# Kernel tuning notes

Measured on AMD Instinct MI355X. Metric: run time of the kernel, lower is better.

The kernel has to match this reference:

```python
import jax, jax.numpy as jnp
import numpy as np

INPUT_DIM, HIDDEN, LATENT, HEADS = 4, 32, 2, 4
N_NODES, N_EDGES = 50000, 800000
EPS_BN = 1e-5
NEG_SLOPE = 0.2


def _glorot(key, shape):
    fan_in, fan_out = shape[0], shape[-1]
    lim = jnp.sqrt(6.0 / (fan_in + fan_out))
    return jax.random.uniform(key, shape, jnp.float32, -lim, lim)


def setup_inputs() -> dict:
    key = jax.random.key(0)
    ks = jax.random.split(key, 20)
    x = jax.random.normal(ks[0], (N_NODES, INPUT_DIM), jnp.float32)
    edge_index = jax.random.randint(ks[1], (2, N_EDGES), 0, N_NODES, jnp.int64)

    def gat_params(k, in_ch, out_ch, heads, concat):
        k1, k2, k3 = jax.random.split(k, 3)
        W = _glorot(k1, (in_ch, heads * out_ch))
        a_src = _glorot(k2, (heads, out_ch))
        a_dst = _glorot(k3, (heads, out_ch))
        b = jnp.zeros((heads * out_ch,) if concat else (out_ch,), jnp.float32)
        return W, a_src, a_dst, b

    w_e1, as_e1, ad_e1, b_e1 = gat_params(ks[2], INPUT_DIM, HIDDEN, HEADS, True)
    w_e3, as_e3, ad_e3, b_e3 = gat_params(ks[3], HIDDEN * HEADS, LATENT, 1, False)
    w_d1, as_d1, ad_d1, b_d1 = gat_params(ks[4], LATENT, HIDDEN, HEADS, True)
    w_d3, as_d3, ad_d3, b_d3 = gat_params(ks[5], HIDDEN * HEADS, INPUT_DIM, 1, False)

    return dict(
        x=x, edge_index=edge_index,
        bn_gamma=jnp.ones((INPUT_DIM,), jnp.float32),
        bn_beta=jnp.zeros((INPUT_DIM,), jnp.float32),
        w_e1=w_e1, as_e1=as_e1, ad_e1=ad_e1, b_e1=b_e1,
        w_e3=w_e3, as_e3=as_e3, ad_e3=ad_e3, b_e3=b_e3,
        w_d1=w_d1, as_d1=as_d1, ad_d1=ad_d1, b_d1=b_d1,
        w_d3=w_d3, as_d3=as_d3, ad_d3=ad_d3, b_d3=b_d3,
    )


def gat_conv(x, src, dst, W, a_src, a_dst, b, heads, out_ch, concat):
    """PyG-style GATConv: gather -> attention -> segment softmax -> scatter."""
    n = x.shape[0]
    h = (x @ W).reshape(n, heads, out_ch)                 # [N,H,C]
    alpha_s = jnp.sum(h * a_src, axis=-1)                 # [N,H]
    alpha_d = jnp.sum(h * a_dst, axis=-1)                 # [N,H]
    e = jax.nn.leaky_relu(alpha_s[src] + alpha_d[dst], NEG_SLOPE)  # [E,H]
    # numerically-stable softmax over incoming edges of each dst node
    m = jax.ops.segment_max(e, dst, num_segments=n)
    e = jnp.exp(e - m[dst])
    s = jax.ops.segment_sum(e, dst, num_segments=n)
    a = e / (s[dst] + 1e-16)                              # [E,H]
    msg = h[src] * a[:, :, None]                          # [E,H,C]
    out = jax.ops.segment_sum(msg, dst, num_segments=n)   # [N,H,C]
    out = out.reshape(n, heads * out_ch) if concat else out.mean(axis=1)
    return out + b


def reference(x, edge_index, bn_gamma, bn_beta,
              w_e1, as_e1, ad_e1, b_e1,
              w_e3, as_e3, ad_e3, b_e3,
              w_d1, as_d1, ad_d1, b_d1,
              w_d3, as_d3, ad_d3, b_d3):
    n = x.shape[0]
    # GATConv default add_self_loops=True
    loops = jnp.arange(n, dtype=edge_index.dtype)
    src = jnp.concatenate([edge_index[0], loops])
    dst = jnp.concatenate([edge_index[1], loops])

    # BatchNorm1d (training-mode batch statistics, biased variance)
    mu = x.mean(axis=0)
    var = x.var(axis=0)
    x_in = (x - mu) * jax.lax.rsqrt(var + EPS_BN) * bn_gamma + bn_beta

    enc1 = jax.nn.relu(gat_conv(x_in, src, dst, w_e1, as_e1, ad_e1, b_e1, HEADS, HIDDEN, True))
    latent = gat_conv(enc1, src, dst, w_e3, as_e3, ad_e3, b_e3, 1, LATENT, False)
    dec1 = jax.nn.relu(gat_conv(latent, src, dst, w_d1, as_d1, ad_d1, b_d1, HEADS, HIDDEN, True))
    x_out = gat_conv(dec1, src, dst, w_d3, as_d3, ad_d3, b_d3, 1, INPUT_DIM, False)
    return x_out
```

## Files before the change

### kernel.cpp

```cpp
#include <hip/hip_runtime.h>

#define NN 50000
#define E0 800000
#define ET 850000
#define EPS_BN 1e-5f
#define SLOPE 0.2f
#define NBP 32
#define EPC 2048
#define NCH 416
#define PBITS 10
#define NP 49
#define SCN (NP*NCH)

__device__ __forceinline__ float lrelu(float v){ return v > 0.f ? v : SLOPE*v; }

__global__ __launch_bounds__(256) void chunk_hist_bn(const int* __restrict__ ei, int* __restrict__ chunkcnt,
                                                     const float* __restrict__ x, float* __restrict__ part){
  __shared__ int cc[NP];
  for (int i=threadIdx.x; i<NP; i+=256) cc[i]=0;
  __syncthreads();
  int base = blockIdx.x*EPC;
  int end = min(base+EPC, ET);
  for (int e = base+threadIdx.x; e < end; e += 256){
    int dst = (e < E0) ? ei[E0 + e] : (e - E0);
    atomicAdd(&cc[dst>>PBITS], 1);
  }
  __syncthreads();
  for (int i=threadIdx.x; i<NP; i+=256) chunkcnt[blockIdx.x*NP + i] = cc[i];

  if (blockIdx.x < NBP){
    float s[4]={0,0,0,0}, q[4]={0,0,0,0};
    for (int n = blockIdx.x*256 + threadIdx.x; n < NN; n += NBP*256){
      float4 v = reinterpret_cast<const float4*>(x)[n];
      s[0]+=v.x; s[1]+=v.y; s[2]+=v.z; s[3]+=v.w;
      q[0]+=v.x*v.x; q[1]+=v.y*v.y; q[2]+=v.z*v.z; q[3]+=v.w*v.w;
    }
    #pragma unroll
    for (int m=1;m<64;m<<=1){
      #pragma unroll
      for (int i=0;i<4;i++){ s[i]+=__shfl_xor(s[i],m); q[i]+=__shfl_xor(q[i],m); }
    }
    __shared__ float lds[4][8];
    int wid = threadIdx.x>>6, lane = threadIdx.x&63;
    if (lane==0){
      #pragma unroll
      for (int i=0;i<4;i++){ lds[wid][i]=s[i]; lds[wid][4+i]=q[i]; }
    }
    __syncthreads();
    if (threadIdx.x < 8){
      float p = lds[0][threadIdx.x]+lds[1][threadIdx.x]+lds[2][threadIdx.x]+lds[3][threadIdx.x];
      part[blockIdx.x*8 + threadIdx.x] = p;
    }
  }
}

__global__ __launch_bounds__(1024) void scan_fold(
    const int* __restrict__ chunkcnt, int* __restrict__ pofs,
    const float* __restrict__ part, const float* __restrict__ gamma, const float* __restrict__ beta,
    const float* __restrict__ w_e1, const float* __restrict__ as_e1, const float* __restrict__ ad_e1,
    const float* __restrict__ w_d1, const float* __restrict__ as_d1, const float* __restrict__ ad_d1,
    float* __restrict__ sclsft, float* __restrict__ fold){
  __shared__ int wsum[1024];
  int t = threadIdx.x;
  const int PER = (SCN + 1023)/1024;
  int vals[PER];
  int mysum = 0;
  #pragma unroll
  for (int k=0;k<PER;k++){
    int idx = t*PER + k;
    int v = 0;
    if (idx < SCN){ int p = idx/NCH, ch = idx - p*NCH; v = chunkcnt[ch*NP + p]; }
    vals[k] = v; mysum += v;
  }
  wsum[t] = mysum; __syncthreads();
  int val = mysum;
  for (int off=1; off<1024; off<<=1){
    int tmp = (t>=off) ? wsum[t-off] : 0;
    __syncthreads();
    val += tmp; wsum[t] = val; __syncthreads();
  }
  int run = val - mysum;
  #pragma unroll
  for (int k=0;k<PER;k++){
    int idx = t*PER + k;
    if (idx < SCN){ int p = idx/NCH, ch = idx - p*NCH; pofs[ch*NP + p] = run; }
    run += vals[k];
  }

  if (t < 64){
    int ch = t&7, bslot = t>>3;
    float s = 0.f;
    for (int b=bslot; b<NBP; b+=8) s += part[b*8 + ch];
    s += __shfl_xor(s,8); s += __shfl_xor(s,16); s += __shfl_xor(s,32);
    float qv = __shfl(s, (t&3)+4);
    if (t < 4){
      float mu  = s*(1.0f/NN);
      float var = qv*(1.0f/NN) - mu*mu;
      float scl = rsqrtf(var + EPS_BN)*gamma[t];
      sclsft[t]   = scl;
      sclsft[4+t] = beta[t] - mu*scl;
    }
  } else if (t < 128){
    int u = t - 64;
    if (u < 32){
      int idx = u & 15; int h = idx>>2; int i = idx&3;
      const float* a = (u<16) ? as_e1 : ad_e1;
      float sum = 0.f;
      for (int c=0;c<32;c++) sum += w_e1[i*128 + h*32 + c] * a[h*32 + c];
      fold[u] = sum;
    } else if (u < 48){
      int idx = u - 32; int j = idx & 7; int h = j>>1; int i = j&1;
      const float* a = (idx<8) ? as_d1 : ad_d1;
      float sum = 0.f;
      for (int c=0;c<32;c++) sum += w_d1[i*128 + h*32 + c] * a[h*32 + c];
      fold[32 + idx] = sum;
    }
  }
}

__global__ __launch_bounds__(256) void partition_pass(const int* __restrict__ ei,
                                                      const int* __restrict__ pofs,
                                                      int2* __restrict__ pedge){
  __shared__ int cur[NP];
  for (int i=threadIdx.x; i<NP; i+=256) cur[i] = pofs[blockIdx.x*NP + i];
  __syncthreads();
  int base = blockIdx.x*EPC;
  int end = min(base+EPC, ET);
  for (int e = base+threadIdx.x; e < end; e += 256){
    int src, dst;
    if (e < E0){ src = ei[e]; dst = ei[E0+e]; } else { src = dst = e - E0; }
    int pos = atomicAdd(&cur[dst>>PBITS], 1);
    pedge[pos] = make_int2(src, dst);
  }
}

__global__ __launch_bounds__(1024) void fine_build(const int2* __restrict__ pedge,
                                                   const int* __restrict__ pofs,
                                                   int* __restrict__ rowptr, int* __restrict__ ssrc){
  int p = blockIdx.x;
  int pstart = pofs[p];
  int pend = (p+1 < NP) ? pofs[p+1] : ET;
  int dbase = p << PBITS;
  __shared__ int hist[1<<PBITS];
  __shared__ int cur[1<<PBITS];
  int t = threadIdx.x;
  hist[t] = 0;
  __syncthreads();
  for (int i = pstart + t; i < pend; i += 1024)
    atomicAdd(&hist[pedge[i].y - dbase], 1);
  __syncthreads();
  int orig = hist[t];
  __syncthreads();
  int v = orig;
  for (int off=1; off<1024; off<<=1){
    int tmp = (t>=off) ? hist[t-off] : 0;
    __syncthreads();
    v += tmp; hist[t] = v; __syncthreads();
  }
  int excl = v - orig;
  int d = dbase + t;
  if (d < NN) rowptr[d] = pstart + excl;
  if (p == NP-1 && t == 0) rowptr[NN] = ET;
  cur[t] = pstart + excl;
  __syncthreads();
  for (int i = pstart + t; i < pend; i += 1024){
    int2 e = pedge[i];
    int pos = atomicAdd(&cur[e.y - dbase], 1);
    ssrc[pos] = e.x;
  }
}

__global__ __launch_bounds__(256) void node1(
    const float* __restrict__ x, const float* __restrict__ sclsft, const float* __restrict__ fold,
    float* __restrict__ pk1, float* __restrict__ ald1){
  int n = blockIdx.x*256 + threadIdx.x;
  if (n >= NN) return;
  float4 v = reinterpret_cast<const float4*>(x)[n];
  float xb[4] = {v.x, v.y, v.z, v.w};
  #pragma unroll
  for (int i=0;i<4;i++) xb[i] = xb[i]*sclsft[i] + sclsft[4+i];
  float4 s4, d4;
  float* sp = &s4.x; float* dp = &d4.x;
  #pragma unroll
  for (int h=0;h<4;h++){
    float s=0.f, d=0.f;
    #pragma unroll
    for (int i=0;i<4;i++){ s += xb[i]*fold[h*4+i]; d += xb[i]*fold[16+h*4+i]; }
    sp[h]=s; dp[h]=d;
  }
  reinterpret_cast<float4*>(pk1)[n*2+0] = s4;
  reinterpret_cast<float4*>(pk1)[n*2+1] = make_float4(xb[0],xb[1],xb[2],xb[3]);
  reinterpret_cast<float4*>(ald1)[n] = d4;
}

__global__ __launch_bounds__(256) void eagg1(
    const float* __restrict__ pk1, const float* __restrict__ ald,
    const int* __restrict__ rowptr, const int* __restrict__ ssrc,
    const float* __restrict__ w_e1, const float* __restrict__ b_e1,
    const float* __restrict__ w_e3, const float* __restrict__ as_e3, const float* __restrict__ ad_e3,
    float* __restrict__ pk2, float* __restrict__ ald2){
  int dst = blockIdx.x*32 + (threadIdx.x>>3);
  int sub = threadIdx.x & 7;
  if (dst >= NN) return;
  int r0 = rowptr[dst], r1 = rowptr[dst+1];
  float4 advv = reinterpret_cast<const float4*>(ald)[dst];
  float adv[4] = {advv.x, advv.y, advv.z, advv.w};
  float sum[4] = {0,0,0,0};
  float acc[4][4] = {{0,0,0,0},{0,0,0,0},{0,0,0,0},{0,0,0,0}};
  for (int i = r0 + sub; i < r1; i += 8){
    int s = ssrc[i];
    float4 a = reinterpret_cast<const float4*>(pk1)[s*2+0];
    float4 f = reinterpret_cast<const float4*>(pk1)[s*2+1];
    float av[4] = {a.x,a.y,a.z,a.w};
    #pragma unroll
    for (int h=0;h<4;h++){
      float w = __expf(lrelu(av[h]+adv[h]));
      sum[h] += w;
      acc[h][0] += w*f.x; acc[h][1] += w*f.y; acc[h][2] += w*f.z; acc[h][3] += w*f.w;
    }
  }
  #pragma unroll
  for (int m=1;m<8;m<<=1){
    #pragma unroll
    for (int h=0;h<4;h++){
      sum[h] += __shfl_xor(sum[h],m);
      #pragma unroll
      for (int c=0;c<4;c++) acc[h][c] += __shfl_xor(acc[h][c],m);
    }
  }
  int hh = sub>>1;
  float G0=acc[0][0], G1=acc[0][1], G2=acc[0][2], G3=acc[0][3], GS=sum[0];
  #pragma unroll
  for (int h=1;h<4;h++){
    if (hh==h){ G0=acc[h][0]; G1=acc[h][1]; G2=acc[h][2]; G3=acc[h][3]; GS=sum[h]; }
  }
  float ginv = 1.f/(GS+1e-16f);
  G0*=ginv; G1*=ginv; G2*=ginv; G3*=ginv;
  float p0 = 0.f, p1 = 0.f;
  int ocb = sub*16;
  #pragma unroll
  for (int q=0;q<4;q++){
    int o = ocb + q*4;
    float4 b  = *reinterpret_cast<const float4*>(b_e1 + o);
    float4 w0 = *reinterpret_cast<const float4*>(w_e1 + 0*128 + o);
    float4 w1 = *reinterpret_cast<const float4*>(w_e1 + 1*128 + o);
    float4 w2 = *reinterpret_cast<const float4*>(w_e1 + 2*128 + o);
    float4 w3 = *reinterpret_cast<const float4*>(w_e1 + 3*128 + o);
    float e0 = fmaxf(b.x + G0*w0.x + G1*w1.x + G2*w2.x + G3*w3.x, 0.f);
    float e1 = fmaxf(b.y + G0*w0.y + G1*w1.y + G2*w2.y + G3*w3.y, 0.f);
    float e2 = fmaxf(b.z + G0*w0.z + G1*w1.z + G2*w2.z + G3*w3.z, 0.f);
    float e3 = fmaxf(b.w + G0*w0.w + G1*w1.w + G2*w2.w + G3*w3.w, 0.f);
    float4 wa = *reinterpret_cast<const float4*>(w_e3 + o*2);
    float4 wb = *reinterpret_cast<const float4*>(w_e3 + o*2 + 4);
    p0 += e0*wa.x + e1*wa.z + e2*wb.x + e3*wb.z;
    p1 += e0*wa.y + e1*wa.w + e2*wb.y + e3*wb.w;
  }
  #pragma unroll
  for (int m=1;m<8;m<<=1){ p0 += __shfl_xor(p0,m); p1 += __shfl_xor(p1,m); }
  if (sub==0){
    reinterpret_cast<float4*>(pk2)[dst] = make_float4(p0, p1, p0*as_e3[0]+p1*as_e3[1], 0.f);
    ald2[dst] = p0*ad_e3[0] + p1*ad_e3[1];
  }
}

__global__ __launch_bounds__(256) void eagg2(
    const float* __restrict__ pk2, const float* __restrict__ ald2,
    const int* __restrict__ rowptr, const int* __restrict__ ssrc,
    const float* __restrict__ b_e3, const float* __restrict__ fold,
    float* __restrict__ pk3, float* __restrict__ ald3){
  int dst = blockIdx.x*32 + (threadIdx.x>>3);
  int sub = threadIdx.x & 7;
  if (dst >= NN) return;
  int r0 = rowptr[dst], r1 = rowptr[dst+1];
  float adv = ald2[dst];
  float sum = 0.f, a0 = 0.f, a1 = 0.f;
  for (int i = r0 + sub; i < r1; i += 8){
    int s = ssrc[i];
    float4 r = reinterpret_cast<const float4*>(pk2)[s];
    float w = __expf(lrelu(r.z + adv));
    sum += w; a0 += w*r.x; a1 += w*r.y;
  }
  #pragma unroll
  for (int m=1;m<8;m<<=1){
    sum += __shfl_xor(sum,m); a0 += __shfl_xor(a0,m); a1 += __shfl_xor(a1,m);
  }
  if (sub != 0) return;
  float inv = 1.f/(sum+1e-16f);
  float l0 = a0*inv + b_e3[0];
  float l1 = a1*inv + b_e3[1];
  float4 s3, d3; float* sp=&s3.x; float* dp=&d3.x;
  #pragma unroll
  for (int h=0;h<4;h++){
    sp[h] = l0*fold[32+h*2+0] + l1*fold[32+h*2+1];
    dp[h] = l0*fold[40+h*2+0] + l1*fold[40+h*2+1];
  }
  reinterpret_cast<float4*>(pk3)[dst*2] = s3;
  pk3[(size_t)dst*8+4] = l0;
  pk3[(size_t)dst*8+5] = l1;
  reinterpret_cast<float4*>(ald3)[dst] = d3;
}

__global__ __launch_bounds__(256) void eagg3(
    const float* __restrict__ pk3, const float* __restrict__ ald3,
    const int* __restrict__ rowptr, const int* __restrict__ ssrc,
    const float* __restrict__ w_d1, const float* __restrict__ b_d1,
    const float* __restrict__ w_d3, const float* __restrict__ as_d3, const float* __restrict__ ad_d3,
    float4* __restrict__ feat4, float* __restrict__ s4a, float* __restrict__ ald4){
  int dst = blockIdx.x*32 + (threadIdx.x>>3);
  int sub = threadIdx.x & 7;
  if (dst >= NN) return;
  int r0 = rowptr[dst], r1 = rowptr[dst+1];
  float4 advv = reinterpret_cast<const float4*>(ald3)[dst];
  float adv[4] = {advv.x, advv.y, advv.z, advv.w};
  float sum[4] = {0,0,0,0};
  float acc[4][2] = {{0,0},{0,0},{0,0},{0,0}};
  for (int i = r0 + sub; i < r1; i += 8){
    int s = ssrc[i];
    float4 a = reinterpret_cast<const float4*>(pk3)[s*2+0];
    float2 f = *reinterpret_cast<const float2*>(pk3 + (size_t)s*8 + 4);
    float av[4] = {a.x,a.y,a.z,a.w};
    #pragma unroll
    for (int h=0;h<4;h++){
      float w = __expf(lrelu(av[h]+adv[h]));
      sum[h] += w;
      acc[h][0] += w*f.x; acc[h][1] += w*f.y;
    }
  }
  #pragma unroll
  for (int m=1;m<8;m<<=1){
    #pragma unroll
    for (int h=0;h<4;h++){
      sum[h] += __shfl_xor(sum[h],m);
      acc[h][0] += __shfl_xor(acc[h][0],m);
      acc[h][1] += __shfl_xor(acc[h][1],m);
    }
  }
  int hh = sub>>1;
  float G0=acc[0][0], G1=acc[0][1], GS=sum[0];
  #pragma unroll
  for (int h=1;h<4;h++){
    if (hh==h){ G0=acc[h][0]; G1=acc[h][1]; GS=sum[h]; }
  }
  float ginv = 1.f/(GS+1e-16f);
  G0*=ginv; G1*=ginv;
  float p0=0.f,p1=0.f,p2=0.f,p3=0.f;
  int ocb = sub*16;
  #pragma unroll
  for (int q=0;q<4;q++){
    int o = ocb + q*4;
    float4 b  = *reinterpret_cast<const float4*>(b_d1 + o);
    float4 w0 = *reinterpret_cast<const float4*>(w_d1 + 0*128 + o);
    float4 w1 = *reinterpret_cast<const float4*>(w_d1 + 1*128 + o);
    float e0 = fmaxf(b.x + G0*w0.x + G1*w1.x, 0.f);
    float e1 = fmaxf(b.y + G0*w0.y + G1*w1.y, 0.f);
    float e2 = fmaxf(b.z + G0*w0.z + G1*w1.z, 0.f);
    float e3 = fmaxf(b.w + G0*w0.w + G1*w1.w, 0.f);
    float4 d0 = *reinterpret_cast<const float4*>(w_d3 + (o+0)*4);
    float4 d1 = *reinterpret_cast<const float4*>(w_d3 + (o+1)*4);
    float4 d2 = *reinterpret_cast<const float4*>(w_d3 + (o+2)*4);
    float4 d3v = *reinterpret_cast<const float4*>(w_d3 + (o+3)*4);
    p0 += e0*d0.x + e1*d1.x + e2*d2.x + e3*d3v.x;
    p1 += e0*d0.y + e1*d1.y + e2*d2.y + e3*d3v.y;
    p2 += e0*d0.z + e1*d1.z + e2*d2.z + e3*d3v.z;
    p3 += e0*d0.w + e1*d1.w + e2*d2.w + e3*d3v.w;
  }
  #pragma unroll
  for (int m=1;m<8;m<<=1){
    p0 += __shfl_xor(p0,m); p1 += __shfl_xor(p1,m);
    p2 += __shfl_xor(p2,m); p3 += __shfl_xor(p3,m);
  }
  if (sub==0){
    feat4[dst] = make_float4(p0,p1,p2,p3);
    s4a[dst]  = p0*as_d3[0]+p1*as_d3[1]+p2*as_d3[2]+p3*as_d3[3];
    ald4[dst] = p0*ad_d3[0]+p1*ad_d3[1]+p2*ad_d3[2]+p3*ad_d3[3];
  }
}

__global__ __launch_bounds__(256) void eagg4(
    const float4* __restrict__ feat4, const float* __restrict__ s4a, const float* __restrict__ ald4,
    const int* __restrict__ rowptr, const int* __restrict__ ssrc,
    const float* __restrict__ b_d3, float* __restrict__ out){
  int dst = blockIdx.x*32 + (threadIdx.x>>3);
  int sub = threadIdx.x & 7;
  if (dst >= NN) return;
  int r0 = rowptr[dst], r1 = rowptr[dst+1];
  float adv = ald4[dst];
  float sum = 0.f, a0=0.f, a1=0.f, a2=0.f, a3=0.f;
  for (int i = r0 + sub; i < r1; i += 8){
    int s = ssrc[i];
    float w = __expf(lrelu(s4a[s] + adv));
    float4 f = feat4[s];
    sum += w; a0 += w*f.x; a1 += w*f.y; a2 += w*f.z; a3 += w*f.w;
  }
  #pragma unroll
  for (int m=1;m<8;m<<=1){
    sum += __shfl_xor(sum,m);
    a0 += __shfl_xor(a0,m); a1 += __shfl_xor(a1,m);
    a2 += __shfl_xor(a2,m); a3 += __shfl_xor(a3,m);
  }
  if (sub != 0) return;
  float inv = 1.f/(sum+1e-16f);
  reinterpret_cast<float4*>(out)[dst] =
    make_float4(a0*inv+b_d3[0], a1*inv+b_d3[1], a2*inv+b_d3[2], a3*inv+b_d3[3]);
}

extern "C" void kernel_launch(void* const* d_in, const int* in_sizes, int n_in,
                              void* d_out, int out_size, void* d_ws, size_t ws_size,
                              hipStream_t stream) {
  const float* x     = (const float*)d_in[0];
  const int*   ei    = (const int*)  d_in[1];
  const float* gamma = (const float*)d_in[2];
  const float* beta  = (const float*)d_in[3];
  const float* w_e1  = (const float*)d_in[4];
  const float* as_e1 = (const float*)d_in[5];
  const float* ad_e1 = (const float*)d_in[6];
  const float* b_e1  = (const float*)d_in[7];
  const float* w_e3  = (const float*)d_in[8];
  const float* as_e3 = (const float*)d_in[9];
  const float* ad_e3 = (const float*)d_in[10];
  const float* b_e3  = (const float*)d_in[11];
  const float* w_d1  = (const float*)d_in[12];
  const float* as_d1 = (const float*)d_in[13];
  const float* ad_d1 = (const float*)d_in[14];
  const float* b_d1  = (const float*)d_in[15];
  const float* w_d3  = (const float*)d_in[16];
  const float* as_d3 = (const float*)d_in[17];
  const float* ad_d3 = (const float*)d_in[18];
  const float* b_d3  = (const float*)d_in[19];

  char* ws = (char*)d_ws;
  size_t off = 0;
  auto alloc = [&](size_t bytes)->void*{
    void* p = ws + off;
    off += (bytes + 255) & ~(size_t)255;
    return p;
  };
  int*   chunkcnt = (int*)  alloc((size_t)NCH*NP*4);
  int*   pofs     = (int*)  alloc((size_t)NCH*NP*4);
  int2*  pedge    = (int2*) alloc((size_t)ET*8);
  int*   rowptr   = (int*)  alloc((size_t)(NN+1)*4);
  int*   ssrc     = (int*)  alloc((size_t)ET*4);
  float* part     = (float*)alloc((size_t)NBP*8*4);
  float* sclsft   = (float*)alloc(32);
  float* fold     = (float*)alloc(64*4);
  float* pk1      = (float*)alloc((size_t)NN*8*4);
  float* ald1     = (float*)alloc((size_t)NN*4*4);
  float* pk2      = (float*)alloc((size_t)NN*4*4);
  float* ald2     = (float*)alloc((size_t)NN*4);
  float* pk3      = (float*)alloc((size_t)NN*8*4);
  float* ald3     = (float*)alloc((size_t)NN*4*4);
  float4* feat4   = (float4*)alloc((size_t)NN*4*4);
  float* s4a      = (float*)alloc((size_t)NN*4);
  float* ald4     = (float*)alloc((size_t)NN*4);

  chunk_hist_bn<<<NCH, 256, 0, stream>>>(ei, chunkcnt, x, part);
  scan_fold<<<1, 1024, 0, stream>>>(chunkcnt, pofs, part, gamma, beta,
                                    w_e1, as_e1, ad_e1, w_d1, as_d1, ad_d1, sclsft, fold);
  partition_pass<<<NCH, 256, 0, stream>>>(ei, pofs, pedge);
  fine_build<<<NP, 1024, 0, stream>>>(pedge, pofs, rowptr, ssrc);

  const int AGG_BLOCKS = (NN+31)/32;

  node1<<<(NN+255)/256, 256, 0, stream>>>(x, sclsft, fold, pk1, ald1);
  eagg1<<<AGG_BLOCKS, 256, 0, stream>>>(pk1, ald1, rowptr, ssrc,
                                        w_e1, b_e1, w_e3, as_e3, ad_e3, pk2, ald2);
  eagg2<<<AGG_BLOCKS, 256, 0, stream>>>(pk2, ald2, rowptr, ssrc, b_e3, fold, pk3, ald3);
  eagg3<<<AGG_BLOCKS, 256, 0, stream>>>(pk3, ald3, rowptr, ssrc,
                                        w_d1, b_d1, w_d3, as_d3, ad_d3, feat4, s4a, ald4);
  eagg4<<<AGG_BLOCKS, 256, 0, stream>>>(feat4, s4a, ald4, rowptr, ssrc, b_d3, (float*)d_out);
}
```

Measured before the change: 127.9 us.

## Drop node1 pass, recompute attention logits on the fly, narrow gather records

Removes the node1 kernel. eagg1 now gathers raw x and applies the batch-norm scale and the folded attention vectors per edge, and later layers store only compact features (float2/float4) while recomputing source and destination logits from them. This cuts per-edge gather bytes and intermediate writes, at the cost of some extra per-edge arithmetic. It also retunes the CSR build to larger chunks, 1024-thread blocks and 512-node partitions, and uses 4 lanes per destination node in place of 8.

Result: faster. 124.1 us (-3.0%).

```diff
diff --git a/kernel.cpp b/kernel.cpp
--- a/kernel.cpp
+++ b/kernel.cpp
@@ -6,31 +6,32 @@
 #define EPS_BN 1e-5f
 #define SLOPE 0.2f
 #define NBP 32
-#define EPC 2048
-#define NCH 416
-#define PBITS 10
-#define NP 49
+#define EPC 8192
+#define NCH 104
+#define PBITS 9
+#define NP 98
 #define SCN (NP*NCH)
 
 __device__ __forceinline__ float lrelu(float v){ return v > 0.f ? v : SLOPE*v; }
 
-__global__ __launch_bounds__(256) void chunk_hist_bn(const int* __restrict__ ei, int* __restrict__ chunkcnt,
-                                                     const float* __restrict__ x, float* __restrict__ part){
+__global__ __launch_bounds__(1024) void chunk_hist_bn(const int* __restrict__ ei, int* __restrict__ chunkcnt,
+                                                      const float* __restrict__ x, float* __restrict__ part){
   __shared__ int cc[NP];
-  for (int i=threadIdx.x; i<NP; i+=256) cc[i]=0;
+  int t = threadIdx.x;
+  for (int i=t; i<NP; i+=1024) cc[i]=0;
   __syncthreads();
   int base = blockIdx.x*EPC;
   int end = min(base+EPC, ET);
-  for (int e = base+threadIdx.x; e < end; e += 256){
+  for (int e = base+t; e < end; e += 1024){
     int dst = (e < E0) ? ei[E0 + e] : (e - E0);
     atomicAdd(&cc[dst>>PBITS], 1);
   }
   __syncthreads();
-  for (int i=threadIdx.x; i<NP; i+=256) chunkcnt[blockIdx.x*NP + i] = cc[i];
+  for (int i=t; i<NP; i+=1024) chunkcnt[blockIdx.x*NP + i] = cc[i];
 
   if (blockIdx.x < NBP){
     float s[4]={0,0,0,0}, q[4]={0,0,0,0};
-    for (int n = blockIdx.x*256 + threadIdx.x; n < NN; n += NBP*256){
+    for (int n = blockIdx.x*1024 + t; n < NN; n += NBP*1024){
       float4 v = reinterpret_cast<const float4*>(x)[n];
       s[0]+=v.x; s[1]+=v.y; s[2]+=v.z; s[3]+=v.w;
       q[0]+=v.x*v.x; q[1]+=v.y*v.y; q[2]+=v.z*v.z; q[3]+=v.w*v.w;
@@ -40,16 +41,18 @@
       #pragma unroll
       for (int i=0;i<4;i++){ s[i]+=__shfl_xor(s[i],m); q[i]+=__shfl_xor(q[i],m); }
     }
-    __shared__ float lds[4][8];
-    int wid = threadIdx.x>>6, lane = threadIdx.x&63;
+    __shared__ float lds[16][8];
+    int wid = t>>6, lane = t&63;
     if (lane==0){
       #pragma unroll
       for (int i=0;i<4;i++){ lds[wid][i]=s[i]; lds[wid][4+i]=q[i]; }
     }
     __syncthreads();
-    if (threadIdx.x < 8){
-      float p = lds[0][threadIdx.x]+lds[1][threadIdx.x]+lds[2][threadIdx.x]+lds[3][threadIdx.x];
-      part[blockIdx.x*8 + threadIdx.x] = p;
+    if (t < 8){
+      float p = 0.f;
+      #pragma unroll
+      for (int w=0;w<16;w++) p += lds[w][t];
+      part[blockIdx.x*8 + t] = p;
     }
   }
 }
@@ -118,15 +121,16 @@
   }
 }
 
-__global__ __launch_bounds__(256) void partition_pass(const int* __restrict__ ei,
-                                                      const int* __restrict__ pofs,
-                                                      int2* __restrict__ pedge){
+__global__ __launch_bounds__(1024) void partition_pass(const int* __restrict__ ei,
+                                                       const int* __restrict__ pofs,
+                                                       int2* __restrict__ pedge){
   __shared__ int cur[NP];
-  for (int i=threadIdx.x; i<NP; i+=256) cur[i] = pofs[blockIdx.x*NP + i];
+  int t = threadIdx.x;
+  for (int i=t; i<NP; i+=1024) cur[i] = pofs[blockIdx.x*NP + i];
   __syncthreads();
   int base = blockIdx.x*EPC;
   int end = min(base+EPC, ET);
-  for (int e = base+threadIdx.x; e < end; e += 256){
+  for (int e = base+t; e < end; e += 1024){
     int src, dst;
     if (e < E0){ src = ei[e]; dst = ei[E0+e]; } else { src = dst = e - E0; }
     int pos = atomicAdd(&cur[dst>>PBITS], 1);
@@ -144,24 +148,27 @@
   __shared__ int hist[1<<PBITS];
   __shared__ int cur[1<<PBITS];
   int t = threadIdx.x;
-  hist[t] = 0;
+  if (t < 512) hist[t] = 0;
   __syncthreads();
   for (int i = pstart + t; i < pend; i += 1024)
     atomicAdd(&hist[pedge[i].y - dbase], 1);
   __syncthreads();
-  int orig = hist[t];
+  int orig = (t < 512) ? hist[t] : 0;
   __syncthreads();
   int v = orig;
-  for (int off=1; off<1024; off<<=1){
-    int tmp = (t>=off) ? hist[t-off] : 0;
+  for (int off=1; off<512; off<<=1){
+    int tmp = (t>=off && t<512) ? hist[t-off] : 0;
     __syncthreads();
-    v += tmp; hist[t] = v; __syncthreads();
-  }
-  int excl = v - orig;
-  int d = dbase + t;
-  if (d < NN) rowptr[d] = pstart + excl;
-  if (p == NP-1 && t == 0) rowptr[NN] = ET;
-  cur[t] = pstart + excl;
+    if (t < 512){ v += tmp; hist[t] = v; }
+    __syncthreads();
+  }
+  if (t < 512){
+    int excl = v - orig;
+    int d = dbase + t;
+    if (d < NN) rowptr[d] = pstart + excl;
+    if (p == NP-1 && t == 0) rowptr[NN] = ET;
+    cur[t] = pstart + excl;
+  }
   __syncthreads();
   for (int i = pstart + t; i < pend; i += 1024){
     int2 e = pedge[i];
@@ -170,57 +177,44 @@
   }
 }
 
-__global__ __launch_bounds__(256) void node1(
+__global__ __launch_bounds__(256) void eagg1(
     const float* __restrict__ x, const float* __restrict__ sclsft, const float* __restrict__ fold,
-    float* __restrict__ pk1, float* __restrict__ ald1){
-  int n = blockIdx.x*256 + threadIdx.x;
-  if (n >= NN) return;
-  float4 v = reinterpret_cast<const float4*>(x)[n];
-  float xb[4] = {v.x, v.y, v.z, v.w};
-  #pragma unroll
-  for (int i=0;i<4;i++) xb[i] = xb[i]*sclsft[i] + sclsft[4+i];
-  float4 s4, d4;
-  float* sp = &s4.x; float* dp = &d4.x;
-  #pragma unroll
-  for (int h=0;h<4;h++){
-    float s=0.f, d=0.f;
-    #pragma unroll
-    for (int i=0;i<4;i++){ s += xb[i]*fold[h*4+i]; d += xb[i]*fold[16+h*4+i]; }
-    sp[h]=s; dp[h]=d;
-  }
-  reinterpret_cast<float4*>(pk1)[n*2+0] = s4;
-  reinterpret_cast<float4*>(pk1)[n*2+1] = make_float4(xb[0],xb[1],xb[2],xb[3]);
-  reinterpret_cast<float4*>(ald1)[n] = d4;
-}
-
-__global__ __launch_bounds__(256) void eagg1(
-    const float* __restrict__ pk1, const float* __restrict__ ald,
     const int* __restrict__ rowptr, const int* __restrict__ ssrc,
-    const float* __restrict__ w_e1, const float* __restrict__ b_e1,
-    const float* __restrict__ w_e3, const float* __restrict__ as_e3, const float* __restrict__ ad_e3,
-    float* __restrict__ pk2, float* __restrict__ ald2){
-  int dst = blockIdx.x*32 + (threadIdx.x>>3);
-  int sub = threadIdx.x & 7;
+    const float* __restrict__ w_e1, const float* __restrict__ b_e1, const float* __restrict__ w_e3,
+    float2* __restrict__ pk2){
+  int dst = blockIdx.x*64 + (threadIdx.x>>2);
+  int sub = threadIdx.x & 3;
   if (dst >= NN) return;
+  float sc[8];
+  #pragma unroll
+  for (int i=0;i<8;i++) sc[i] = sclsft[i];
+  float fs[16];
+  #pragma unroll
+  for (int i=0;i<16;i++) fs[i] = fold[i];
+  float4 xd = reinterpret_cast<const float4*>(x)[dst];
+  float xbd[4] = {xd.x*sc[0]+sc[4], xd.y*sc[1]+sc[5], xd.z*sc[2]+sc[6], xd.w*sc[3]+sc[7]};
+  float ald[4];
+  #pragma unroll
+  for (int h=0;h<4;h++)
+    ald[h] = xbd[0]*fold[16+h*4+0] + xbd[1]*fold[16+h*4+1]
+           + xbd[2]*fold[16+h*4+2] + xbd[3]*fold[16+h*4+3];
   int r0 = rowptr[dst], r1 = rowptr[dst+1];
-  float4 advv = reinterpret_cast<const float4*>(ald)[dst];
-  float adv[4] = {advv.x, advv.y, advv.z, advv.w};
   float sum[4] = {0,0,0,0};
   float acc[4][4] = {{0,0,0,0},{0,0,0,0},{0,0,0,0},{0,0,0,0}};
-  for (int i = r0 + sub; i < r1; i += 8){
+  for (int i = r0 + sub; i < r1; i += 4){
     int s = ssrc[i];
-    float4 a = reinterpret_cast<const float4*>(pk1)[s*2+0];
-    float4 f = reinterpret_cast<const float4*>(pk1)[s*2+1];
-    float av[4] = {a.x,a.y,a.z,a.w};
+    float4 xs = reinterpret_cast<const float4*>(x)[s];
+    float xb[4] = {xs.x*sc[0]+sc[4], xs.y*sc[1]+sc[5], xs.z*sc[2]+sc[6], xs.w*sc[3]+sc[7]};
     #pragma unroll
     for (int h=0;h<4;h++){
-      float w = __expf(lrelu(av[h]+adv[h]));
+      float a = xb[0]*fs[h*4+0] + xb[1]*fs[h*4+1] + xb[2]*fs[h*4+2] + xb[3]*fs[h*4+3];
+      float w = __expf(lrelu(a + ald[h]));
       sum[h] += w;
-      acc[h][0] += w*f.x; acc[h][1] += w*f.y; acc[h][2] += w*f.z; acc[h][3] += w*f.w;
-    }
-  }
-  #pragma unroll
-  for (int m=1;m<8;m<<=1){
+      acc[h][0] += w*xb[0]; acc[h][1] += w*xb[1]; acc[h][2] += w*xb[2]; acc[h][3] += w*xb[3];
+    }
+  }
+  #pragma unroll
+  for (int m=1;m<4;m<<=1){
     #pragma unroll
     for (int h=0;h<4;h++){
       sum[h] += __shfl_xor(sum[h],m);
@@ -228,19 +222,18 @@
       for (int c=0;c<4;c++) acc[h][c] += __shfl_xor(acc[h][c],m);
     }
   }
-  int hh = sub>>1;
   float G0=acc[0][0], G1=acc[0][1], G2=acc[0][2], G3=acc[0][3], GS=sum[0];
   #pragma unroll
   for (int h=1;h<4;h++){
-    if (hh==h){ G0=acc[h][0]; G1=acc[h][1]; G2=acc[h][2]; G3=acc[h][3]; GS=sum[h]; }
-  }
-  float ginv = 1.f/(GS+1e-16f);
-  G0*=ginv; G1*=ginv; G2*=ginv; G3*=ginv;
+    if (sub==h){ G0=acc[h][0]; G1=acc[h][1]; G2=acc[h][2]; G3=acc[h][3]; GS=sum[h]; }
+  }
+  float inv = 1.f/(GS+1e-16f);
+  G0*=inv; G1*=inv; G2*=inv; G3*=inv;
   float p0 = 0.f, p1 = 0.f;
-  int ocb = sub*16;
-  #pragma unroll
-  for (int q=0;q<4;q++){
-    int o = ocb + q*4;
+  int ob = sub*32;
+  #pragma unroll
+  for (int q=0;q<8;q++){
+    int o = ob + q*4;
     float4 b  = *reinterpret_cast<const float4*>(b_e1 + o);
     float4 w0 = *reinterpret_cast<const float4*>(w_e1 + 0*128 + o);
     float4 w1 = *reinterpret_cast<const float4*>(w_e1 + 1*128 + o);
@@ -255,79 +248,71 @@
     p0 += e0*wa.x + e1*wa.z + e2*wb.x + e3*wb.z;
     p1 += e0*wa.y + e1*wa.w + e2*wb.y + e3*wb.w;
   }
-  #pragma unroll
-  for (int m=1;m<8;m<<=1){ p0 += __shfl_xor(p0,m); p1 += __shfl_xor(p1,m); }
+  p0 += __shfl_xor(p0,1); p0 += __shfl_xor(p0,2);
+  p1 += __shfl_xor(p1,1); p1 += __shfl_xor(p1,2);
+  if (sub==0) pk2[dst] = make_float2(p0, p1);
+}
+
+__global__ __launch_bounds__(256) void eagg2(
+    const float2* __restrict__ pk2,
+    const int* __restrict__ rowptr, const int* __restrict__ ssrc,
+    const float* __restrict__ as_e3, const float* __restrict__ ad_e3, const float* __restrict__ b_e3,
+    float2* __restrict__ lat2){
+  int dst = blockIdx.x*64 + (threadIdx.x>>2);
+  int sub = threadIdx.x & 3;
+  if (dst >= NN) return;
+  float as0 = as_e3[0], as1 = as_e3[1];
+  float2 pd = pk2[dst];
+  float adv = pd.x*ad_e3[0] + pd.y*ad_e3[1];
+  int r0 = rowptr[dst], r1 = rowptr[dst+1];
+  float sum = 0.f, a0 = 0.f, a1 = 0.f;
+  for (int i = r0 + sub; i < r1; i += 4){
+    int s = ssrc[i];
+    float2 p = pk2[s];
+    float w = __expf(lrelu(p.x*as0 + p.y*as1 + adv));
+    sum += w; a0 += w*p.x; a1 += w*p.y;
+  }
+  #pragma unroll
+  for (int m=1;m<4;m<<=1){
+    sum += __shfl_xor(sum,m); a0 += __shfl_xor(a0,m); a1 += __shfl_xor(a1,m);
+  }
   if (sub==0){
-    reinterpret_cast<float4*>(pk2)[dst] = make_float4(p0, p1, p0*as_e3[0]+p1*as_e3[1], 0.f);
-    ald2[dst] = p0*ad_e3[0] + p1*ad_e3[1];
-  }
-}
-
-__global__ __launch_bounds__(256) void eagg2(
-    const float* __restrict__ pk2, const float* __restrict__ ald2,
+    float inv = 1.f/(sum+1e-16f);
+    lat2[dst] = make_float2(a0*inv + b_e3[0], a1*inv + b_e3[1]);
+  }
+}
+
+__global__ __launch_bounds__(256) void eagg3(
+    const float2* __restrict__ lat2, const float* __restrict__ fold,
     const int* __restrict__ rowptr, const int* __restrict__ ssrc,
-    const float* __restrict__ b_e3, const float* __restrict__ fold,
-    float* __restrict__ pk3, float* __restrict__ ald3){
-  int dst = blockIdx.x*32 + (threadIdx.x>>3);
-  int sub = threadIdx.x & 7;
+    const float* __restrict__ w_d1, const float* __restrict__ b_d1, const float* __restrict__ w_d3,
+    float4* __restrict__ pk4){
+  int dst = blockIdx.x*64 + (threadIdx.x>>2);
+  int sub = threadIdx.x & 3;
   if (dst >= NN) return;
+  float f3[8];
+  #pragma unroll
+  for (int i=0;i<8;i++) f3[i] = fold[32+i];
+  float2 ld = lat2[dst];
+  float ald[4];
+  #pragma unroll
+  for (int h=0;h<4;h++) ald[h] = ld.x*fold[40+h*2+0] + ld.y*fold[40+h*2+1];
   int r0 = rowptr[dst], r1 = rowptr[dst+1];
-  float adv = ald2[dst];
-  float sum = 0.f, a0 = 0.f, a1 = 0.f;
-  for (int i = r0 + sub; i < r1; i += 8){
-    int s = ssrc[i];
-    float4 r = reinterpret_cast<const float4*>(pk2)[s];
-    float w = __expf(lrelu(r.z + adv));
-    sum += w; a0 += w*r.x; a1 += w*r.y;
-  }
-  #pragma unroll
-  for (int m=1;m<8;m<<=1){
-    sum += __shfl_xor(sum,m); a0 += __shfl_xor(a0,m); a1 += __shfl_xor(a1,m);
-  }
-  if (sub != 0) return;
-  float inv = 1.f/(sum+1e-16f);
-  float l0 = a0*inv + b_e3[0];
-  float l1 = a1*inv + b_e3[1];
-  float4 s3, d3; float* sp=&s3.x; float* dp=&d3.x;
-  #pragma unroll
-  for (int h=0;h<4;h++){
-    sp[h] = l0*fold[32+h*2+0] + l1*fold[32+h*2+1];
-    dp[h] = l0*fold[40+h*2+0] + l1*fold[40+h*2+1];
-  }
-  reinterpret_cast<float4*>(pk3)[dst*2] = s3;
-  pk3[(size_t)dst*8+4] = l0;
-  pk3[(size_t)dst*8+5] = l1;
-  reinterpret_cast<float4*>(ald3)[dst] = d3;
-}
-
-__global__ __launch_bounds__(256) void eagg3(
-    const float* __restrict__ pk3, const float* __restrict__ ald3,
-    const int* __restrict__ rowptr, const int* __restrict__ ssrc,
-    const float* __restrict__ w_d1, const float* __restrict__ b_d1,
-    const float* __restrict__ w_d3, const float* __restrict__ as_d3, const float* __restrict__ ad_d3,
-    float4* __restrict__ feat4, float* __restrict__ s4a, float* __restrict__ ald4){
-  int dst = blockIdx.x*32 + (threadIdx.x>>3);
-  int sub = threadIdx.x & 7;
-  if (dst >= NN) return;
-  int r0 = rowptr[dst], r1 = rowptr[dst+1];
-  float4 advv = reinterpret_cast<const float4*>(ald3)[dst];
-  float adv[4] = {advv.x, advv.y, advv.z, advv.w};
   float sum[4] = {0,0,0,0};
   float acc[4][2] = {{0,0},{0,0},{0,0},{0,0}};
-  for (int i = r0 + sub; i < r1; i += 8){
+  for (int i = r0 + sub; i < r1; i += 4){
     int s = ssrc[i];
-    float4 a = reinterpret_cast<const float4*>(pk3)[s*2+0];
-    float2 f = *reinterpret_cast<const float2*>(pk3 + (size_t)s*8 + 4);
-    float av[4] = {a.x,a.y,a.z,a.w};
+    float2 l = lat2[s];
     #pragma unroll
     for (int h=0;h<4;h++){
-      float w = __expf(lrelu(av[h]+adv[h]));
+      float a = l.x*f3[h*2+0] + l.y*f3[h*2+1];
+      float w = __expf(lrelu(a + ald[h]));
       sum[h] += w;
-      acc[h][0] += w*f.x; acc[h][1] += w*f.y;
-    }
-  }
-  #pragma unroll
-  for (int m=1;m<8;m<<=1){
+      acc[h][0] += w*l.x; acc[h][1] += w*l.y;
+    }
+  }
+  #pragma unroll
+  for (int m=1;m<4;m<<=1){
     #pragma unroll
     for (int h=0;h<4;h++){
       sum[h] += __shfl_xor(sum[h],m);
@@ -335,19 +320,18 @@
       acc[h][1] += __shfl_xor(acc[h][1],m);
     }
   }
-  int hh = sub>>1;
   float G0=acc[0][0], G1=acc[0][1], GS=sum[0];
   #pragma unroll
   for (int h=1;h<4;h++){
-    if (hh==h){ G0=acc[h][0]; G1=acc[h][1]; GS=sum[h]; }
-  }
-  float ginv = 1.f/(GS+1e-16f);
-  G0*=ginv; G1*=ginv;
+    if (sub==h){ G0=acc[h][0]; G1=acc[h][1]; GS=sum[h]; }
+  }
+  float inv = 1.f/(GS+1e-16f);
+  G0*=inv; G1*=inv;
   float p0=0.f,p1=0.f,p2=0.f,p3=0.f;
-  int ocb = sub*16;
-  #pragma unroll
-  for (int q=0;q<4;q++){
-    int o = ocb + q*4;
+  int ob = sub*32;
+  #pragma unroll
+  for (int q=0;q<8;q++){
+    int o = ob + q*4;
     float4 b  = *reinterpret_cast<const float4*>(b_d1 + o);
     float4 w0 = *reinterpret_cast<const float4*>(w_d1 + 0*128 + o);
     float4 w1 = *reinterpret_cast<const float4*>(w_d1 + 1*128 + o);
@@ -358,50 +342,50 @@
     float4 d0 = *reinterpret_cast<const float4*>(w_d3 + (o+0)*4);
     float4 d1 = *reinterpret_cast<const float4*>(w_d3 + (o+1)*4);
     float4 d2 = *reinterpret_cast<const float4*>(w_d3 + (o+2)*4);
-    float4 d3v = *reinterpret_cast<const float4*>(w_d3 + (o+3)*4);
+    float4 d3v= *reinterpret_cast<const float4*>(w_d3 + (o+3)*4);
     p0 += e0*d0.x + e1*d1.x + e2*d2.x + e3*d3v.x;
     p1 += e0*d0.y + e1*d1.y + e2*d2.y + e3*d3v.y;
     p2 += e0*d0.z + e1*d1.z + e2*d2.z + e3*d3v.z;
     p3 += e0*d0.w + e1*d1.w + e2*d2.w + e3*d3v.w;
   }
   #pragma unroll
-  for (int m=1;m<8;m<<=1){
+  for (int m=1;m<4;m<<=1){
     p0 += __shfl_xor(p0,m); p1 += __shfl_xor(p1,m);
     p2 += __shfl_xor(p2,m); p3 += __shfl_xor(p3,m);
   }
-  if (sub==0){
-    feat4[dst] = make_float4(p0,p1,p2,p3);
-    s4a[dst]  = p0*as_d3[0]+p1*as_d3[1]+p2*as_d3[2]+p3*as_d3[3];
-    ald4[dst] = p0*ad_d3[0]+p1*ad_d3[1]+p2*ad_d3[2]+p3*ad_d3[3];
-  }
+  if (sub==0) pk4[dst] = make_float4(p0,p1,p2,p3);
 }
 
 __global__ __launch_bounds__(256) void eagg4(
-    const float4* __restrict__ feat4, const float* __restrict__ s4a, const float* __restrict__ ald4,
+    const float4* __restrict__ pk4,
     const int* __restrict__ rowptr, const int* __restrict__ ssrc,
-    const float* __restrict__ b_d3, float* __restrict__ out){
-  int dst = blockIdx.x*32 + (threadIdx.x>>3);
-  int sub = threadIdx.x & 7;
+    const float* __restrict__ as_d3, const float* __restrict__ ad_d3, const float* __restrict__ b_d3,
+    float* __restrict__ out){
+  int dst = blockIdx.x*64 + (threadIdx.x>>2);
+  int sub = threadIdx.x & 3;
   if (dst >= NN) return;
+  float as0=as_d3[0], as1=as_d3[1], as2=as_d3[2], as3=as_d3[3];
+  float4 hd = pk4[dst];
+  float adv = hd.x*ad_d3[0] + hd.y*ad_d3[1] + hd.z*ad_d3[2] + hd.w*ad_d3[3];
   int r0 = rowptr[dst], r1 = rowptr[dst+1];
-  float adv = ald4[dst];
   float sum = 0.f, a0=0.f, a1=0.f, a2=0.f, a3=0.f;
-  for (int i = r0 + sub; i < r1; i += 8){
+  for (int i = r0 + sub; i < r1; i += 4){
     int s = ssrc[i];
-    float w = __expf(lrelu(s4a[s] + adv));
-    float4 f = feat4[s];
+    float4 f = pk4[s];
+    float w = __expf(lrelu(f.x*as0 + f.y*as1 + f.z*as2 + f.w*as3 + adv));
     sum += w; a0 += w*f.x; a1 += w*f.y; a2 += w*f.z; a3 += w*f.w;
   }
   #pragma unroll
-  for (int m=1;m<8;m<<=1){
+  for (int m=1;m<4;m<<=1){
     sum += __shfl_xor(sum,m);
     a0 += __shfl_xor(a0,m); a1 += __shfl_xor(a1,m);
     a2 += __shfl_xor(a2,m); a3 += __shfl_xor(a3,m);
   }
-  if (sub != 0) return;
-  float inv = 1.f/(sum+1e-16f);
-  reinterpret_cast<float4*>(out)[dst] =
-    make_float4(a0*inv+b_d3[0], a1*inv+b_d3[1], a2*inv+b_d3[2], a3*inv+b_d3[3]);
+  if (sub==0){
+    float inv = 1.f/(sum+1e-16f);
+    reinterpret_cast<float4*>(out)[dst] =
+      make_float4(a0*inv+b_d3[0], a1*inv+b_d3[1], a2*inv+b_d3[2], a3*inv+b_d3[3]);
+  }
 }
 
 extern "C" void kernel_launch(void* const* d_in, const int* in_sizes, int n_in,
@@ -435,37 +419,28 @@
     off += (bytes + 255) & ~(size_t)255;
     return p;
   };
-  int*   chunkcnt = (int*)  alloc((size_t)NCH*NP*4);
-  int*   pofs     = (int*)  alloc((size_t)NCH*NP*4);
-  int2*  pedge    = (int2*) alloc((size_t)ET*8);
-  int*   rowptr   = (int*)  alloc((size_t)(NN+1)*4);
-  int*   ssrc     = (int*)  alloc((size_t)ET*4);
-  float* part     = (float*)alloc((size_t)NBP*8*4);
-  float* sclsft   = (float*)alloc(32);
-  float* fold     = (float*)alloc(64*4);
-  float* pk1      = (float*)alloc((size_t)NN*8*4);
-  float* ald1     = (float*)alloc((size_t)NN*4*4);
-  float* pk2      = (float*)alloc((size_t)NN*4*4);
-  float* ald2     = (float*)alloc((size_t)NN*4);
-  float* pk3      = (float*)alloc((size_t)NN*8*4);
-  float* ald3     = (float*)alloc((size_t)NN*4*4);
-  float4* feat4   = (float4*)alloc((size_t)NN*4*4);
-  float* s4a      = (float*)alloc((size_t)NN*4);
-  float* ald4     = (float*)alloc((size_t)NN*4);
-
-  chunk_hist_bn<<<NCH, 256, 0, stream>>>(ei, chunkcnt, x, part);
+  int*    chunkcnt = (int*)   alloc((size_t)SCN*4);
+  int*    pofs     = (int*)   alloc((size_t)SCN*4);
+  int2*   pedge    = (int2*)  alloc((size_t)ET*8);
+  int*    rowptr   = (int*)   alloc((size_t)(NN+1)*4);
+  int*    ssrc     = (int*)   alloc((size_t)ET*4);
+  float*  part     = (float*) alloc((size_t)NBP*8*4);
+  float*  sclsft   = (float*) alloc(32);
+  float*  fold     = (float*) alloc(64*4);
+  float2* pk2      = (float2*)alloc((size_t)NN*8);
+  float2* lat2     = (float2*)alloc((size_t)NN*8);
+  float4* pk4      = (float4*)alloc((size_t)NN*16);
+
+  chunk_hist_bn<<<NCH, 1024, 0, stream>>>(ei, chunkcnt, x, part);
   scan_fold<<<1, 1024, 0, stream>>>(chunkcnt, pofs, part, gamma, beta,
                                     w_e1, as_e1, ad_e1, w_d1, as_d1, ad_d1, sclsft, fold);
-  partition_pass<<<NCH, 256, 0, stream>>>(ei, pofs, pedge);
+  partition_pass<<<NCH, 1024, 0, stream>>>(ei, pofs, pedge);
   fine_build<<<NP, 1024, 0, stream>>>(pedge, pofs, rowptr, ssrc);
 
-  const int AGG_BLOCKS = (NN+31)/32;
-
-  node1<<<(NN+255)/256, 256, 0, stream>>>(x, sclsft, fold, pk1, ald1);
-  eagg1<<<AGG_BLOCKS, 256, 0, stream>>>(pk1, ald1, rowptr, ssrc,
-                                        w_e1, b_e1, w_e3, as_e3, ad_e3, pk2, ald2);
-  eagg2<<<AGG_BLOCKS, 256, 0, stream>>>(pk2, ald2, rowptr, ssrc, b_e3, fold, pk3, ald3);
-  eagg3<<<AGG_BLOCKS, 256, 0, stream>>>(pk3, ald3, rowptr, ssrc,
-                                        w_d1, b_d1, w_d3, as_d3, ad_d3, feat4, s4a, ald4);
-  eagg4<<<AGG_BLOCKS, 256, 0, stream>>>(feat4, s4a, ald4, rowptr, ssrc, b_d3, (float*)d_out);
-}
+  const int NAGG = (NN + 63)/64;
+
+  eagg1<<<NAGG, 256, 0, stream>>>(x, sclsft, fold, rowptr, ssrc, w_e1, b_e1, w_e3, pk2);
+  eagg2<<<NAGG, 256, 0, stream>>>(pk2, rowptr, ssrc, as_e3, ad_e3, b_e3, lat2);
+  eagg3<<<NAGG, 256, 0, stream>>>(lat2, fold, rowptr, ssrc, w_d1, b_d1, w_d3, pk4);
+  eagg4<<<NAGG, 256, 0, stream>>>(pk4, rowptr, ssrc, as_d3, ad_d3, b_d3, (float*)d_out);
+}
```
